# Kernel tuning notes

Measured on AMD Instinct MI355X. Metric: run time of the kernel, lower is better.

## Reference

```python
import jax, jax.numpy as jnp
import numpy as np

B, S, F = 4, 2048, 256
H, D = 8, 32            # n_heads, width_embedding; H*D == F
LN_EPS = 1e-3           # tf.keras LayerNormalization default epsilon


def setup_inputs() -> dict:
    key = jax.random.key(0)
    ks = jax.random.split(key, 6)
    s = 1.0 / np.sqrt(F)
    return {
        "x": jax.random.normal(ks[0], (B, S, F), dtype=jnp.float32),
        "Wq": jax.random.normal(ks[1], (F, H * D), dtype=jnp.float32) * s,
        "Wk": jax.random.normal(ks[2], (F, H * D), dtype=jnp.float32) * s,
        "Wv": jax.random.normal(ks[3], (F, H * D), dtype=jnp.float32) * s,
        "Wf": jax.random.normal(ks[4], (H * D, F), dtype=jnp.float32) * s,
        "bf": jnp.zeros((F,), dtype=jnp.float32),
    }


def reference(x, Wq, Wk, Wv, Wf, bf):
    # QKV projections (no bias), split heads: [B,S,H*D] -> [B,H,S,D]
    def split(t):
        return t.reshape(B, S, H, D).transpose(0, 2, 1, 3)

    q = split(x @ Wq) / jnp.sqrt(jnp.asarray(H, x.dtype))  # NOTE: module scales by sqrt(n_heads)
    k = split(x @ Wk)
    v = split(x @ Wv)

    scores = jnp.einsum("bhsd,bhtd->bhst", q, k)          # [B,H,S,S]
    attn = jax.nn.softmax(scores, axis=-1)
    ctx = jnp.einsum("bhst,bhtd->bhsd", attn, v)           # [B,H,S,D]

    y = ctx.transpose(0, 2, 1, 3).reshape(B, S, H * D)     # merge heads
    y = jax.nn.relu(y @ Wf + bf)                            # final dense with relu

    # residual + LayerNorm(center=False, scale=False)
    z = x + y
    mean = jnp.mean(z, axis=-1, keepdims=True)
    var = jnp.var(z, axis=-1, keepdims=True)
    return (z - mean) * jax.lax.rsqrt(var + LN_EPS)
```

## Files before the change

### kernel.cpp

```cpp
#include <hip/hip_runtime.h>
#include <math.h>

#define NB 4
#define NS 2048
#define NF 256
#define NH 8
#define ND 32

constexpr float LN_EPS = 1e-3f;
constexpr float QSCALE = 0.35355339059327373f;
constexpr float LOG2E  = 1.4426950408889634f;

typedef __bf16 bf16x8 __attribute__((ext_vector_type(8)));
typedef float f32x4 __attribute__((ext_vector_type(4)));

__global__ __launch_bounds__(256)
void prep(const float* __restrict__ x, const float* __restrict__ Wq,
          const float* __restrict__ Wk, const float* __restrict__ Wv,
          const float* __restrict__ Wf, unsigned short* __restrict__ xb,
          unsigned short* __restrict__ wt)
{
    __shared__ float tile[64][65];
    const int id = blockIdx.x;
    const int t = threadIdx.x;

    if (id < 1024) {
        const int i = (id * 256 + t) * 8;
        float4 a = *(const float4*)(x + i);
        float4 b = *(const float4*)(x + i + 4);
        union { ushort4 u; __bf16 h[4]; } o0, o1;
        o0.h[0] = (__bf16)a.x; o0.h[1] = (__bf16)a.y; o0.h[2] = (__bf16)a.z; o0.h[3] = (__bf16)a.w;
        o1.h[0] = (__bf16)b.x; o1.h[1] = (__bf16)b.y; o1.h[2] = (__bf16)b.z; o1.h[3] = (__bf16)b.w;
        *(ushort4*)(xb + i) = o0.u;
        *(ushort4*)(xb + i + 4) = o1.u;
        return;
    }

    const int wid = id - 1024;
    const int z = wid >> 4;
    const int tl = wid & 15;
    const float* W = (z == 0) ? Wq : (z == 1) ? Wk : (z == 2) ? Wv : Wf;
    const float scale = (z == 0) ? QSCALE * LOG2E : 1.0f;
    const int r0 = (tl >> 2) * 64, c0 = (tl & 3) * 64;
    const int tr = t >> 4, tc4 = (t & 15) * 4;

    #pragma unroll
    for (int p = 0; p < 4; ++p) {
        float4 v = *(const float4*)(W + (size_t)(r0 + tr + p * 16) * NF + c0 + tc4);
        tile[tr + p * 16][tc4 + 0] = v.x;
        tile[tr + p * 16][tc4 + 1] = v.y;
        tile[tr + p * 16][tc4 + 2] = v.z;
        tile[tr + p * 16][tc4 + 3] = v.w;
    }
    __syncthreads();
    #pragma unroll
    for (int p = 0; p < 4; ++p) {
        union { ushort4 u; __bf16 h[4]; } o;
        #pragma unroll
        for (int j = 0; j < 4; ++j)
            o.h[j] = (__bf16)(tile[tc4 + j][tr + p * 16] * scale);
        *(ushort4*)(wt + (size_t)z * 65536 + (size_t)(c0 + tr + p * 16) * NF + r0 + tc4) = o.u;
    }
}

__global__ __launch_bounds__(256)
void qkv_mfma(const unsigned short* __restrict__ xb, const unsigned short* __restrict__ wt,
              unsigned short* __restrict__ qo, unsigned short* __restrict__ ko,
              unsigned short* __restrict__ vo)
{
    const int z = blockIdx.y;
    unsigned short* out = (z == 0) ? qo : (z == 1) ? ko : vo;
    const unsigned short* W = wt + (size_t)z * 65536;

    const int r0 = blockIdx.x * 64;
    const int t = threadIdx.x;
    const int w = t >> 6, lane = t & 63;
    const int l15 = lane & 15, lhi = lane >> 4;
    const int wr = w >> 1, wc = w & 1;

    f32x4 acc[2][8] = {};

    for (int kt = 0; kt < NF; kt += 32) {
        bf16x8 a0 = *(const bf16x8*)(xb + (size_t)(r0 + wr * 32 + l15) * NF + kt + lhi * 8);
        bf16x8 a1 = *(const bf16x8*)(xb + (size_t)(r0 + wr * 32 + 16 + l15) * NF + kt + lhi * 8);
        #pragma unroll
        for (int c = 0; c < 8; ++c) {
            bf16x8 b = *(const bf16x8*)(W + (size_t)(wc * 128 + c * 16 + l15) * NF + kt + lhi * 8);
            acc[0][c] = __builtin_amdgcn_mfma_f32_16x16x32_bf16(a0, b, acc[0][c], 0, 0, 0);
            acc[1][c] = __builtin_amdgcn_mfma_f32_16x16x32_bf16(a1, b, acc[1][c], 0, 0, 0);
        }
    }

    #pragma unroll
    for (int i = 0; i < 2; ++i) {
        #pragma unroll
        for (int c = 0; c < 8; ++c) {
            const int col = wc * 128 + c * 16 + l15;
            const int h = col >> 5, d = col & 31;
            #pragma unroll
            for (int r = 0; r < 4; ++r) {
                const int row = r0 + wr * 32 + i * 16 + lhi * 4 + r;
                const int b = row >> 11, s = row & 2047;
                __bf16 o = (__bf16)acc[i][c][r];
                out[((size_t)(b * NH + h) * NS + s) * ND + d] = *(unsigned short*)&o;
            }
        }
    }
}

__global__ __launch_bounds__(256)
void attn_mfma(const unsigned short* __restrict__ q, const unsigned short* __restrict__ k,
               const unsigned short* __restrict__ v, unsigned short* __restrict__ ctxb)
{
    const int bh = blockIdx.x;
    const int s0 = blockIdx.y * 64;
    const int t = threadIdx.x;
    const int w = t >> 6;
    const int lane = t & 63;
    const int l15 = lane & 15;
    const int lhi = lane >> 4;

    __shared__ unsigned short ps[4][16][72];
    __shared__ unsigned short vt[2][32][72];

    const unsigned short* qb = q + (size_t)bh * NS * ND;
    const unsigned short* kb = k + (size_t)bh * NS * ND;
    const unsigned short* vb = v + (size_t)bh * NS * ND;

    bf16x8 qfrag = *(const bf16x8*)(qb + (size_t)(s0 + w * 16 + l15) * ND + lhi * 8);

    float lpart = 0.0f;
    f32x4 acc0 = {0.f, 0.f, 0.f, 0.f};
    f32x4 acc1 = {0.f, 0.f, 0.f, 0.f};

    bf16x8 kf[4], kn[4];
    #pragma unroll
    for (int f = 0; f < 4; ++f)
        kf[f] = *(const bf16x8*)(kb + (size_t)(f * 16 + l15) * ND + lhi * 8);
    {
        bf16x8 vv = *(const bf16x8*)(vb + (size_t)lane * ND + w * 8);
        union { bf16x8 v8; unsigned short s[8]; } u; u.v8 = vv;
        #pragma unroll
        for (int i = 0; i < 8; ++i) vt[0][w * 8 + i][lane] = u.s[i];
    }
    __syncthreads();

    int cur = 0;
    for (int tI = 0; tI < 32; ++tI) {
        const int ktn = ((tI + 1) & 31) * 64;
        bf16x8 vv = *(const bf16x8*)(vb + (size_t)(ktn + lane) * ND + w * 8);
        #pragma unroll
        for (int f = 0; f < 4; ++f)
            kn[f] = *(const bf16x8*)(kb + (size_t)(ktn + f * 16 + l15) * ND + lhi * 8);

        const f32x4 zero = {0.f, 0.f, 0.f, 0.f};
        f32x4 sc[4];
        __builtin_amdgcn_s_setprio(1);
        #pragma unroll
        for (int f = 0; f < 4; ++f)
            sc[f] = __builtin_amdgcn_mfma_f32_16x16x32_bf16(kf[f], qfrag, zero, 0, 0, 0);
        __builtin_amdgcn_s_setprio(0);

        #pragma unroll
        for (int f = 0; f < 4; ++f) {
            float p0 = __builtin_amdgcn_exp2f(sc[f][0]);
            float p1 = __builtin_amdgcn_exp2f(sc[f][1]);
            float p2 = __builtin_amdgcn_exp2f(sc[f][2]);
            float p3 = __builtin_amdgcn_exp2f(sc[f][3]);
            lpart += (p0 + p1) + (p2 + p3);
            union { ushort4 u; __bf16 h[4]; } pk;
            pk.h[0] = (__bf16)p0; pk.h[1] = (__bf16)p1;
            pk.h[2] = (__bf16)p2; pk.h[3] = (__bf16)p3;
            *(ushort4*)&ps[w][l15][f * 16 + lhi * 4] = pk.u;
        }

        __builtin_amdgcn_s_setprio(1);
        #pragma unroll
        for (int c = 0; c < 2; ++c) {
            bf16x8 pa  = *(const bf16x8*)&ps[w][l15][c * 32 + lhi * 8];
            bf16x8 vf0 = *(const bf16x8*)&vt[cur][l15][c * 32 + lhi * 8];
            bf16x8 vf1 = *(const bf16x8*)&vt[cur][16 + l15][c * 32 + lhi * 8];
            acc0 = __builtin_amdgcn_mfma_f32_16x16x32_bf16(pa, vf0, acc0, 0, 0, 0);
            acc1 = __builtin_amdgcn_mfma_f32_16x16x32_bf16(pa, vf1, acc1, 0, 0, 0);
        }
        __builtin_amdgcn_s_setprio(0);

        {
            union { bf16x8 v8; unsigned short s[8]; } u; u.v8 = vv;
            #pragma unroll
            for (int i = 0; i < 8; ++i) vt[cur ^ 1][w * 8 + i][lane] = u.s[i];
        }
        #pragma unroll
        for (int f = 0; f < 4; ++f) kf[f] = kn[f];
        __syncthreads();
        cur ^= 1;
    }

    lpart += __shfl_xor(lpart, 16);
    lpart += __shfl_xor(lpart, 32);

    const int b = bh >> 3, h = bh & 7;
    #pragma unroll
    for (int r = 0; r < 4; ++r) {
        float li = __shfl(lpart, lhi * 4 + r);
        float inv = 1.0f / li;
        int row = s0 + w * 16 + lhi * 4 + r;
        unsigned short* op = ctxb + ((size_t)b * NS + row) * NF + h * ND;
        __bf16 o0 = (__bf16)(acc0[r] * inv);
        __bf16 o1 = (__bf16)(acc1[r] * inv);
        op[l15]      = *(unsigned short*)&o0;
        op[16 + l15] = *(unsigned short*)&o1;
    }
}

__global__ __launch_bounds__(256)
void dense_ln(const unsigned short* __restrict__ ctxb, const unsigned short* __restrict__ wft,
              const float* __restrict__ bfp, const float* __restrict__ x,
              float* __restrict__ out)
{
    const int r0 = blockIdx.x * 32;
    const int t = threadIdx.x;
    const int w = t >> 6;
    const int lane = t & 63;
    const int l15 = lane & 15;
    const int lhi = lane >> 4;

    __shared__ float zs[32][258];

    f32x4 acc[2][4] = {};

    for (int kt = 0; kt < NF; kt += 32) {
        bf16x8 a0 = *(const bf16x8*)(ctxb + (size_t)(r0 + l15) * NF + kt + lhi * 8);
        bf16x8 a1 = *(const bf16x8*)(ctxb + (size_t)(r0 + 16 + l15) * NF + kt + lhi * 8);
        #pragma unroll
        for (int c = 0; c < 4; ++c) {
            bf16x8 b = *(const bf16x8*)(wft + (size_t)(w * 64 + c * 16 + l15) * NF + kt + lhi * 8);
            acc[0][c] = __builtin_amdgcn_mfma_f32_16x16x32_bf16(a0, b, acc[0][c], 0, 0, 0);
            acc[1][c] = __builtin_amdgcn_mfma_f32_16x16x32_bf16(a1, b, acc[1][c], 0, 0, 0);
        }
    }

    #pragma unroll
    for (int i = 0; i < 2; ++i) {
        #pragma unroll
        for (int c = 0; c < 4; ++c) {
            const int col = w * 64 + c * 16 + l15;
            const float bb = bfp[col];
            #pragma unroll
            for (int r = 0; r < 4; ++r) {
                const int row = i * 16 + lhi * 4 + r;
                zs[row][col] = fmaxf(acc[i][c][r] + bb, 0.0f);
            }
        }
    }
    __syncthreads();

    #pragma unroll
    for (int i = 0; i < 8; ++i) {
        const int row = w * 8 + i;
        float4 yv = *(const float4*)&zs[row][lane * 4];
        float4 xv = *(const float4*)(x + (size_t)(r0 + row) * NF + lane * 4);
        float z0 = xv.x + yv.x, z1 = xv.y + yv.y;
        float z2 = xv.z + yv.z, z3 = xv.w + yv.w;
        float sum = z0 + z1 + z2 + z3;
        float sq  = z0*z0 + z1*z1 + z2*z2 + z3*z3;
        #pragma unroll
        for (int o = 1; o < 64; o <<= 1) {
            sum += __shfl_xor(sum, o);
            sq  += __shfl_xor(sq, o);
        }
        float mean = sum * (1.0f / NF);
        float var  = sq * (1.0f / NF) - mean * mean;
        float rstd = rsqrtf(var + LN_EPS);
        float4 o4;
        o4.x = (z0 - mean) * rstd;
        o4.y = (z1 - mean) * rstd;
        o4.z = (z2 - mean) * rstd;
        o4.w = (z3 - mean) * rstd;
        *(float4*)(out + (size_t)(r0 + row) * NF + lane * 4) = o4;
    }
}

extern "C" void kernel_launch(void* const* d_in, const int* in_sizes, int n_in,
                              void* d_out, int out_size, void* d_ws, size_t ws_size,
                              hipStream_t stream)
{
    const float* x  = (const float*)d_in[0];
    const float* Wq = (const float*)d_in[1];
    const float* Wk = (const float*)d_in[2];
    const float* Wv = (const float*)d_in[3];
    const float* Wf = (const float*)d_in[4];
    const float* bf = (const float*)d_in[5];
    float* out = (float*)d_out;

    const size_t per = (size_t)NB * NH * NS * ND;
    unsigned short* q    = (unsigned short*)d_ws;
    unsigned short* kk   = q + per;
    unsigned short* vv   = kk + per;
    unsigned short* xb   = vv + per;
    unsigned short* wt   = xb + per;
    unsigned short* ctxb = wt + 4 * 65536;

    prep<<<dim3(1024 + 64), 256, 0, stream>>>(x, Wq, Wk, Wv, Wf, xb, wt);
    qkv_mfma<<<dim3(128, 3), 256, 0, stream>>>(xb, wt, q, kk, vv);
    attn_mfma<<<dim3(NB * NH, NS / 64), 256, 0, stream>>>(q, kk, vv, ctxb);
    dense_ln<<<dim3((NB * NS) / 32), 256, 0, stream>>>(ctxb, wt + 3 * 65536, bf, x, out);
}
```

Before: 88.89 us.

## Fuse x bf16 conversion into QKV GEMM and software-pipeline attention QK^T

Drops the separate x-to-bf16 pass from the prep kernel, so the QKV projection now reads fp32 x directly and converts it in registers. The attention loop computes QK^T scores one tile ahead and prefetches K two tiles ahead, so the score MFMAs overlap with the exp/PV work of the previous tile. Unroll-by-2 pragmas are added to the GEMM loops. In exchange, the QKV kernel reads twice the bytes for x (once per z block, three times in total), and the attention loop holds more registers.

```diff
diff --git a/kernel.cpp b/kernel.cpp
--- a/kernel.cpp
+++ b/kernel.cpp
@@ -15,28 +15,13 @@
 typedef float f32x4 __attribute__((ext_vector_type(4)));
 
 __global__ __launch_bounds__(256)
-void prep(const float* __restrict__ x, const float* __restrict__ Wq,
-          const float* __restrict__ Wk, const float* __restrict__ Wv,
-          const float* __restrict__ Wf, unsigned short* __restrict__ xb,
-          unsigned short* __restrict__ wt)
+void prep_w(const float* __restrict__ Wq, const float* __restrict__ Wk,
+            const float* __restrict__ Wv, const float* __restrict__ Wf,
+            unsigned short* __restrict__ wt)
 {
     __shared__ float tile[64][65];
-    const int id = blockIdx.x;
+    const int wid = blockIdx.x;
     const int t = threadIdx.x;
-
-    if (id < 1024) {
-        const int i = (id * 256 + t) * 8;
-        float4 a = *(const float4*)(x + i);
-        float4 b = *(const float4*)(x + i + 4);
-        union { ushort4 u; __bf16 h[4]; } o0, o1;
-        o0.h[0] = (__bf16)a.x; o0.h[1] = (__bf16)a.y; o0.h[2] = (__bf16)a.z; o0.h[3] = (__bf16)a.w;
-        o1.h[0] = (__bf16)b.x; o1.h[1] = (__bf16)b.y; o1.h[2] = (__bf16)b.z; o1.h[3] = (__bf16)b.w;
-        *(ushort4*)(xb + i) = o0.u;
-        *(ushort4*)(xb + i + 4) = o1.u;
-        return;
-    }
-
-    const int wid = id - 1024;
     const int z = wid >> 4;
     const int tl = wid & 15;
     const float* W = (z == 0) ? Wq : (z == 1) ? Wk : (z == 2) ? Wv : Wf;
@@ -64,7 +49,7 @@
 }
 
 __global__ __launch_bounds__(256)
-void qkv_mfma(const unsigned short* __restrict__ xb, const unsigned short* __restrict__ wt,
+void qkv_mfma(const float* __restrict__ x, const unsigned short* __restrict__ wt,
               unsigned short* __restrict__ qo, unsigned short* __restrict__ ko,
               unsigned short* __restrict__ vo)
 {
@@ -80,9 +65,19 @@
 
     f32x4 acc[2][8] = {};
 
+    #pragma unroll 2
     for (int kt = 0; kt < NF; kt += 32) {
-        bf16x8 a0 = *(const bf16x8*)(xb + (size_t)(r0 + wr * 32 + l15) * NF + kt + lhi * 8);
-        bf16x8 a1 = *(const bf16x8*)(xb + (size_t)(r0 + wr * 32 + 16 + l15) * NF + kt + lhi * 8);
+        const float* xr0 = x + (size_t)(r0 + wr * 32 + l15) * NF + kt + lhi * 8;
+        const float* xr1 = x + (size_t)(r0 + wr * 32 + 16 + l15) * NF + kt + lhi * 8;
+        float4 f00 = *(const float4*)xr0;
+        float4 f01 = *(const float4*)(xr0 + 4);
+        float4 f10 = *(const float4*)xr1;
+        float4 f11 = *(const float4*)(xr1 + 4);
+        bf16x8 a0, a1;
+        a0[0] = (__bf16)f00.x; a0[1] = (__bf16)f00.y; a0[2] = (__bf16)f00.z; a0[3] = (__bf16)f00.w;
+        a0[4] = (__bf16)f01.x; a0[5] = (__bf16)f01.y; a0[6] = (__bf16)f01.z; a0[7] = (__bf16)f01.w;
+        a1[0] = (__bf16)f10.x; a1[1] = (__bf16)f10.y; a1[2] = (__bf16)f10.z; a1[3] = (__bf16)f10.w;
+        a1[4] = (__bf16)f11.x; a1[5] = (__bf16)f11.y; a1[6] = (__bf16)f11.z; a1[7] = (__bf16)f11.w;
         #pragma unroll
         for (int c = 0; c < 8; ++c) {
             bf16x8 b = *(const bf16x8*)(W + (size_t)(wc * 128 + c * 16 + l15) * NF + kt + lhi * 8);
@@ -133,11 +128,18 @@
     f32x4 acc0 = {0.f, 0.f, 0.f, 0.f};
     f32x4 acc1 = {0.f, 0.f, 0.f, 0.f};
 
-    bf16x8 kf[4], kn[4];
-    #pragma unroll
-    for (int f = 0; f < 4; ++f)
-        kf[f] = *(const bf16x8*)(kb + (size_t)(f * 16 + l15) * ND + lhi * 8);
+    const f32x4 zero = {0.f, 0.f, 0.f, 0.f};
+    f32x4 sc[4];
+    bf16x8 kf[4];
     {
+        #pragma unroll
+        for (int f = 0; f < 4; ++f) {
+            bf16x8 k0 = *(const bf16x8*)(kb + (size_t)(f * 16 + l15) * ND + lhi * 8);
+            sc[f] = __builtin_amdgcn_mfma_f32_16x16x32_bf16(k0, qfrag, zero, 0, 0, 0);
+        }
+        #pragma unroll
+        for (int f = 0; f < 4; ++f)
+            kf[f] = *(const bf16x8*)(kb + (size_t)(64 + f * 16 + l15) * ND + lhi * 8);
         bf16x8 vv = *(const bf16x8*)(vb + (size_t)lane * ND + w * 8);
         union { bf16x8 v8; unsigned short s[8]; } u; u.v8 = vv;
         #pragma unroll
@@ -146,33 +148,37 @@
     __syncthreads();
 
     int cur = 0;
+    #pragma unroll 2
     for (int tI = 0; tI < 32; ++tI) {
-        const int ktn = ((tI + 1) & 31) * 64;
+        const int ktn  = ((tI + 1) & 31) * 64;
+        const int ktn2 = ((tI + 2) & 31) * 64;
         bf16x8 vv = *(const bf16x8*)(vb + (size_t)(ktn + lane) * ND + w * 8);
+        bf16x8 kn[4];
         #pragma unroll
         for (int f = 0; f < 4; ++f)
-            kn[f] = *(const bf16x8*)(kb + (size_t)(ktn + f * 16 + l15) * ND + lhi * 8);
-
-        const f32x4 zero = {0.f, 0.f, 0.f, 0.f};
-        f32x4 sc[4];
+            kn[f] = *(const bf16x8*)(kb + (size_t)(ktn2 + f * 16 + l15) * ND + lhi * 8);
+
+        f32x4 scn[4];
         __builtin_amdgcn_s_setprio(1);
         #pragma unroll
         for (int f = 0; f < 4; ++f)
-            sc[f] = __builtin_amdgcn_mfma_f32_16x16x32_bf16(kf[f], qfrag, zero, 0, 0, 0);
+            scn[f] = __builtin_amdgcn_mfma_f32_16x16x32_bf16(kf[f], qfrag, zero, 0, 0, 0);
         __builtin_amdgcn_s_setprio(0);
 
+        float lp[4];
         #pragma unroll
         for (int f = 0; f < 4; ++f) {
             float p0 = __builtin_amdgcn_exp2f(sc[f][0]);
             float p1 = __builtin_amdgcn_exp2f(sc[f][1]);
             float p2 = __builtin_amdgcn_exp2f(sc[f][2]);
             float p3 = __builtin_amdgcn_exp2f(sc[f][3]);
-            lpart += (p0 + p1) + (p2 + p3);
             union { ushort4 u; __bf16 h[4]; } pk;
             pk.h[0] = (__bf16)p0; pk.h[1] = (__bf16)p1;
             pk.h[2] = (__bf16)p2; pk.h[3] = (__bf16)p3;
             *(ushort4*)&ps[w][l15][f * 16 + lhi * 4] = pk.u;
-        }
+            lp[f] = (p0 + p1) + (p2 + p3);
+        }
+        lpart += (lp[0] + lp[1]) + (lp[2] + lp[3]);
 
         __builtin_amdgcn_s_setprio(1);
         #pragma unroll
@@ -192,6 +198,8 @@
         }
         #pragma unroll
         for (int f = 0; f < 4; ++f) kf[f] = kn[f];
+        #pragma unroll
+        for (int f = 0; f < 4; ++f) sc[f] = scn[f];
         __syncthreads();
         cur ^= 1;
     }
@@ -229,6 +237,7 @@
 
     f32x4 acc[2][4] = {};
 
+    #pragma unroll 2
     for (int kt = 0; kt < NF; kt += 32) {
         bf16x8 a0 = *(const bf16x8*)(ctxb + (size_t)(r0 + l15) * NF + kt + lhi * 8);
         bf16x8 a1 = *(const bf16x8*)(ctxb + (size_t)(r0 + 16 + l15) * NF + kt + lhi * 8);
@@ -297,12 +306,11 @@
     unsigned short* q    = (unsigned short*)d_ws;
     unsigned short* kk   = q + per;
     unsigned short* vv   = kk + per;
-    unsigned short* xb   = vv + per;
-    unsigned short* wt   = xb + per;
+    unsigned short* wt   = vv + per;
     unsigned short* ctxb = wt + 4 * 65536;
 
-    prep<<<dim3(1024 + 64), 256, 0, stream>>>(x, Wq, Wk, Wv, Wf, xb, wt);
-    qkv_mfma<<<dim3(128, 3), 256, 0, stream>>>(xb, wt, q, kk, vv);
+    prep_w<<<dim3(64), 256, 0, stream>>>(Wq, Wk, Wv, Wf, wt);
+    qkv_mfma<<<dim3(128, 3), 256, 0, stream>>>(x, wt, q, kk, vv);
     attn_mfma<<<dim3(NB * NH, NS / 64), 256, 0, stream>>>(q, kk, vv, ctxb);
     dense_ln<<<dim3((NB * NS) / 32), 256, 0, stream>>>(ctxb, wt + 3 * 65536, bf, x, out);
 }
```

New measurement: 87.81 us. About the same (-1.2%).
